# Optimization experiments

Measured on AMD Instinct MI355X. Metric: run time of the kernel, lower is better.

Reference implementation:

```python
import jax, jax.numpy as jnp
import numpy as np
from jax import lax

SR = 4      # sr_prior
LAM = 0.1   # lam

# ---- MATLAB-style bicubic imresize (as used by the DRP repo's imresize) ----

def _cubic(x):
    ax = np.abs(x); ax2 = ax * ax; ax3 = ax2 * ax
    return ((1.5 * ax3 - 2.5 * ax2 + 1.0) * (ax <= 1)
            + (-0.5 * ax3 + 2.5 * ax2 - 4.0 * ax + 2.0) * ((ax > 1) & (ax <= 2)))

def _resize_matrix(in_len, out_len, scale):
    """Dense (out_len, in_len) bicubic resize matrix with antialiasing on downscale."""
    kw = 4.0
    if scale < 1.0:
        kw = kw / scale  # antialias: widen kernel
    x = np.arange(1, out_len + 1, dtype=np.float64)
    u = x / scale + 0.5 * (1.0 - 1.0 / scale)
    left = np.floor(u - kw / 2.0)
    P = int(np.ceil(kw)) + 2
    ind = left[:, None] + np.arange(P)[None, :]
    if scale < 1.0:
        w = scale * _cubic(scale * (u[:, None] - ind))
    else:
        w = _cubic(u[:, None] - ind)
    w = w / w.sum(axis=1, keepdims=True)
    # mirror boundary handling (MATLAB imresize)
    aux = np.concatenate([np.arange(in_len), np.arange(in_len - 1, -1, -1)])
    idx = aux[np.mod(ind.astype(np.int64) - 1, aux.size)]
    W = np.zeros((out_len, in_len), dtype=np.float64)
    rows = np.repeat(np.arange(out_len), P)
    np.add.at(W, (rows, idx.ravel()), w.ravel())
    return W.astype(np.float32)

def _imresize(img, scale):
    # img: (C, H, W) -> (C, H*scale, W*scale), separable matrix form
    C, H, W = img.shape
    oh, ow = int(round(H * scale)), int(round(W * scale))
    Wh = jnp.asarray(_resize_matrix(H, oh, scale))
    Ww = jnp.asarray(_resize_matrix(W, ow, scale))
    t = jnp.einsum('oi,cij->coj', Wh, img)      # resize rows
    return jnp.einsum('pj,coj->cop', Ww, t)     # resize cols

def _wrap_corr(x, k):
    """Cross-correlate (C,H,W) with 2D kernel k under circular ('wrap') padding."""
    ph, pw = k.shape[0] // 2, k.shape[1] // 2
    xp = jnp.pad(x, ((0, 0), (ph, ph), (pw, pw)), mode='wrap')
    y = lax.conv_general_dilated(xp[:, None, :, :], k[None, None, :, :], (1, 1), 'VALID')
    return y[:, 0]


def setup_inputs() -> dict:
    key = jax.random.key(0)
    k1, k2 = jax.random.split(key)
    im = jax.random.normal(k1, (1, 3, 2048, 2048), dtype=jnp.float32)
    kernel = jax.random.uniform(k2, (25, 25), dtype=jnp.float32)
    kernel = kernel / kernel.sum()  # normalized blur PSF
    return {"im": im, "kernel": kernel}


def reference(im, kernel):
    x = im[0]  # (C, H, W)
    # ndimage.convolve(x, k, wrap)  == correlate with flipped kernel
    ax = _wrap_corr(x, kernel[::-1, ::-1])
    # ndimage.convolve(ax, k[::-1,::-1], wrap) == correlate with k (adjoint A^T)
    atax = _wrap_corr(ax, kernel)
    hx = _imresize(x, 1.0 / SR)       # H x: downsample
    hthx = _imresize(hx, float(SR))   # H^T(ish): upsample back
    return (atax + LAM * hthx)[None]  # (1, C, H, W)
```

## Files before the change

kernel.cpp:

```cpp
#include <hip/hip_runtime.h>

static constexpr int IMG  = 2048;
static constexpr int CH   = 3;
static constexpr int KS   = 25;
static constexpr int HALO = 12;
static constexpr int DN   = 512;
static constexpr int PD   = 18;
static constexpr int PU   = 6;
static constexpr float LAM = 0.1f;

__device__ __forceinline__ double cubic_d(double x) {
  double ax = fabs(x), ax2 = ax * ax, ax3 = ax2 * ax;
  if (ax <= 1.0) return 1.5 * ax3 - 2.5 * ax2 + 1.0;
  if (ax <= 2.0) return -0.5 * ax3 + 2.5 * ax2 - 4.0 * ax + 2.0;
  return 0.0;
}

__global__ void build_tables(float* dwW, int* dwI, float* uwW, int* uwI) {
  int i = blockIdx.x * blockDim.x + threadIdx.x;
  if (i < DN) {
    const double scale = 0.25;
    double u = (double)(i + 1) / scale + 0.5 * (1.0 - 1.0 / scale);
    double left = floor(u - 8.0);
    double w[PD]; int id[PD]; double s = 0.0;
    for (int p = 0; p < PD; ++p) {
      double ind = left + p;
      w[p] = scale * cubic_d(scale * (u - ind));
      s += w[p];
      long long m = ((long long)ind - 1) % (2 * IMG);
      if (m < 0) m += 2 * IMG;
      id[p] = (m < IMG) ? (int)m : (int)(2 * IMG - 1 - m);
    }
    for (int p = 0; p < PD; ++p) {
      dwW[i * PD + p] = (float)(w[p] / s);
      dwI[i * PD + p] = id[p];
    }
  }
  if (i < IMG) {
    const double scale = 4.0;
    double u = (double)(i + 1) / scale + 0.5 * (1.0 - 1.0 / scale);
    double left = floor(u - 2.0);
    double w[PU]; int id[PU]; double s = 0.0;
    for (int p = 0; p < PU; ++p) {
      double ind = left + p;
      w[p] = cubic_d(u - ind);
      s += w[p];
      long long m = ((long long)ind - 1) % (2 * DN);
      if (m < 0) m += 2 * DN;
      id[p] = (m < DN) ? (int)m : (int)(2 * DN - 1 - m);
    }
    for (int p = 0; p < PU; ++p) {
      uwW[i * PU + p] = (float)(w[p] / s);
      uwI[i * PU + p] = id[p];
    }
  }
}

template <int FLIP>
__global__ __launch_bounds__(256, 4) void corr25(const float* __restrict__ src,
                                                 const float* __restrict__ kw,
                                                 float* __restrict__ dst) {
  constexpr int TW = 128, TH = 32;
  constexpr int SW = 160;
  constexpr int SH = TH + KS - 1;
  constexpr int CHUNKS = 152 / 4;
  __shared__ float tile[SH][SW];

  const int tid = threadIdx.x;
  const int c   = blockIdx.z;
  const int x0  = blockIdx.x * TW;
  const int y0  = blockIdx.y * TH;
  const float* s = src + (size_t)c * IMG * IMG;

  const bool xwrap = (x0 < HALO) || (x0 + TW + HALO > IMG);
  for (int ci = tid; ci < SH * CHUNKS; ci += 256) {
    int r  = ci / CHUNKS;
    int cj = ci - r * CHUNKS;
    int gy = (y0 + r - HALO) & (IMG - 1);
    int col  = 4 * cj;
    int scol = col ^ (((r >> 1) & 7) << 2);
    float4 v;
    if (!xwrap) {
      v = *reinterpret_cast<const float4*>(&s[(size_t)gy * IMG + (x0 - HALO + col)]);
    } else {
      int gx = x0 - HALO + col;
      v.x = s[(size_t)gy * IMG + ((gx + 0) & (IMG - 1))];
      v.y = s[(size_t)gy * IMG + ((gx + 1) & (IMG - 1))];
      v.z = s[(size_t)gy * IMG + ((gx + 2) & (IMG - 1))];
      v.w = s[(size_t)gy * IMG + ((gx + 3) & (IMG - 1))];
    }
    *reinterpret_cast<float4*>(&tile[r][scol]) = v;
  }
  __syncthreads();

  const int tx    = tid & 15;
  const int tyt   = tid >> 4;
  const int ox    = tx * 8;
  const int rbase = tyt * 2;

  float acc0[8], acc1[8];
#pragma unroll
  for (int o = 0; o < 8; ++o) { acc0[o] = 0.f; acc1[o] = 0.f; }

#pragma unroll 2
  for (int rr = 0; rr < KS + 1; ++rr) {
    const int r   = rbase + rr;
    const int swz = ((r >> 1) & 7) << 2;
    float row[32];
#pragma unroll
    for (int j = 0; j < 8; ++j) {
      float4 v = *reinterpret_cast<const float4*>(&tile[r][(ox + 4 * j) ^ swz]);
      row[4 * j + 0] = v.x; row[4 * j + 1] = v.y;
      row[4 * j + 2] = v.z; row[4 * j + 3] = v.w;
    }
    if (rr <= KS - 1) {
      const int ky = rr;
#pragma unroll
      for (int kx = 0; kx < KS; ++kx) {
        float w = FLIP ? kw[(KS - 1 - ky) * KS + (KS - 1 - kx)]
                       : kw[ky * KS + kx];
#pragma unroll
        for (int o = 0; o < 8; ++o) acc0[o] = fmaf(w, row[kx + o], acc0[o]);
      }
    }
    if (rr >= 1) {
      const int ky = rr - 1;
#pragma unroll
      for (int kx = 0; kx < KS; ++kx) {
        float w = FLIP ? kw[(KS - 1 - ky) * KS + (KS - 1 - kx)]
                       : kw[ky * KS + kx];
#pragma unroll
        for (int o = 0; o < 8; ++o) acc1[o] = fmaf(w, row[kx + o], acc1[o]);
      }
    }
  }

  float* d0 = dst + (size_t)c * IMG * IMG + (size_t)(y0 + rbase) * IMG + x0 + ox;
  *reinterpret_cast<float4*>(d0)           = make_float4(acc0[0], acc0[1], acc0[2], acc0[3]);
  *reinterpret_cast<float4*>(d0 + 4)       = make_float4(acc0[4], acc0[5], acc0[6], acc0[7]);
  *reinterpret_cast<float4*>(d0 + IMG)     = make_float4(acc1[0], acc1[1], acc1[2], acc1[3]);
  *reinterpret_cast<float4*>(d0 + IMG + 4) = make_float4(acc1[4], acc1[5], acc1[6], acc1[7]);
}

__global__ void rows_down(const float* __restrict__ src, float* __restrict__ dst,
                          const float* __restrict__ wW, const int* __restrict__ wI) {
  int x = blockIdx.x * blockDim.x + threadIdx.x;
  int o = blockIdx.y;
  int c = blockIdx.z;
  const float* s = src + (size_t)c * IMG * IMG;
  float acc = 0.f;
#pragma unroll
  for (int p = 0; p < PD; ++p)
    acc = fmaf(wW[o * PD + p], s[(size_t)wI[o * PD + p] * IMG + x], acc);
  dst[((size_t)c * DN + o) * IMG + x] = acc;
}

__global__ void cols_down(const float* __restrict__ src, float* __restrict__ dst,
                          const float* __restrict__ wW, const int* __restrict__ wI) {
  int o = blockIdx.x * blockDim.x + threadIdx.x;
  int y = blockIdx.y;
  int c = blockIdx.z;
  const float* s = src + ((size_t)c * DN + y) * IMG;
  float acc = 0.f;
#pragma unroll
  for (int p = 0; p < PD; ++p)
    acc = fmaf(wW[o * PD + p], s[wI[o * PD + p]], acc);
  dst[((size_t)c * DN + y) * DN + o] = acc;
}

__global__ void rows_up(const float* __restrict__ src, float* __restrict__ dst,
                        const float* __restrict__ wW, const int* __restrict__ wI) {
  int x = blockIdx.x * blockDim.x + threadIdx.x;
  int o = blockIdx.y;
  int c = blockIdx.z;
  const float* s = src + (size_t)c * DN * DN;
  float acc = 0.f;
#pragma unroll
  for (int p = 0; p < PU; ++p)
    acc = fmaf(wW[o * PU + p], s[(size_t)wI[o * PU + p] * DN + x], acc);
  dst[((size_t)c * IMG + o) * DN + x] = acc;
}

__global__ void cols_up_add(const float* __restrict__ src, float* __restrict__ out,
                            const float* __restrict__ wW, const int* __restrict__ wI) {
  int x = blockIdx.x * blockDim.x + threadIdx.x;
  int y = blockIdx.y;
  int c = blockIdx.z;
  const float* s = src + ((size_t)c * IMG + y) * DN;
  float acc = 0.f;
#pragma unroll
  for (int p = 0; p < PU; ++p)
    acc = fmaf(wW[x * PU + p], s[wI[x * PU + p]], acc);
  size_t oi = ((size_t)c * IMG + y) * IMG + x;
  out[oi] = fmaf(LAM, acc, out[oi]);
}

extern "C" void kernel_launch(void* const* d_in, const int* in_sizes, int n_in,
                              void* d_out, int out_size, void* d_ws, size_t ws_size,
                              hipStream_t stream) {
  const float* im  = (const float*)d_in[0];
  const float* ker = (const float*)d_in[1];
  float* out = (float*)d_out;
  float* ws  = (float*)d_ws;

  const size_t NIM = (size_t)CH * IMG * IMG;

  float* ax = ws;
  float* t1 = ws;
  float* t2 = t1 + (size_t)CH * DN * IMG;
  float* t3 = t2 + (size_t)CH * DN * DN;
  float* dwW = ws + NIM;
  int*   dwI = (int*)(dwW + DN * PD);
  float* uwW = (float*)(dwI + DN * PD);
  int*   uwI = (int*)(uwW + (size_t)IMG * PU);

  build_tables<<<(IMG + 255) / 256, 256, 0, stream>>>(dwW, dwI, uwW, uwI);

  dim3 cgrid(IMG / 128, IMG / 32, CH);
  corr25<1><<<cgrid, 256, 0, stream>>>(im, ker, ax);
  corr25<0><<<cgrid, 256, 0, stream>>>(ax, ker, out);

  rows_down  <<<dim3(IMG / 256, DN,  CH), 256, 0, stream>>>(im, t1, dwW, dwI);
  cols_down  <<<dim3(DN  / 256, DN,  CH), 256, 0, stream>>>(t1, t2, dwW, dwI);
  rows_up    <<<dim3(DN  / 256, IMG, CH), 256, 0, stream>>>(t2, t3, uwW, uwI);
  cols_up_add<<<dim3(IMG / 256, IMG, CH), 256, 0, stream>>>(t3, out, uwW, uwI);
}
```

Measured before the change: 471.9 us.

## Register-block four output rows per thread and double-buffer LDS strip loads

The 25x25 correlation tile grows from 32 to 64 rows, and each thread now accumulates 4 output rows instead of 2. Each loaded LDS strip therefore feeds up to four accumulator rows, which cuts shared-memory reads and halo overhead per output. Strip loads are double-buffered so the next row is fetched while FMAs run on the current one, and the LDS swizzle is adjusted to the new row grouping. In exchange, register pressure rises and launch bounds drop to 2 blocks per CU, which lowers occupancy.

```diff
diff --git a/kernel.cpp b/kernel.cpp
--- a/kernel.cpp
+++ b/kernel.cpp
@@ -57,13 +57,14 @@
 }
 
 template <int FLIP>
-__global__ __launch_bounds__(256, 4) void corr25(const float* __restrict__ src,
-                                                 const float* __restrict__ kw,
+__global__ __launch_bounds__(256, 2) void corr25(const float* __restrict__ src,
+                                                 const float* __restrict__ kwp,
                                                  float* __restrict__ dst) {
-  constexpr int TW = 128, TH = 32;
+  constexpr int TW = 128, TH = 64;
   constexpr int SW = 160;
   constexpr int SH = TH + KS - 1;
   constexpr int CHUNKS = 152 / 4;
+  constexpr int NSTRIP = 4 + KS - 1;
   __shared__ float tile[SH][SW];
 
   const int tid = threadIdx.x;
@@ -78,7 +79,7 @@
     int cj = ci - r * CHUNKS;
     int gy = (y0 + r - HALO) & (IMG - 1);
     int col  = 4 * cj;
-    int scol = col ^ (((r >> 1) & 7) << 2);
+    int scol = col ^ (((r >> 2) & 7) << 2);
     float4 v;
     if (!xwrap) {
       v = *reinterpret_cast<const float4*>(&s[(size_t)gy * IMG + (x0 - HALO + col)]);
@@ -96,50 +97,63 @@
   const int tx    = tid & 15;
   const int tyt   = tid >> 4;
   const int ox    = tx * 8;
-  const int rbase = tyt * 2;
-
-  float acc0[8], acc1[8];
-#pragma unroll
-  for (int o = 0; o < 8; ++o) { acc0[o] = 0.f; acc1[o] = 0.f; }
-
-#pragma unroll 2
-  for (int rr = 0; rr < KS + 1; ++rr) {
-    const int r   = rbase + rr;
-    const int swz = ((r >> 1) & 7) << 2;
-    float row[32];
-#pragma unroll
-    for (int j = 0; j < 8; ++j) {
-      float4 v = *reinterpret_cast<const float4*>(&tile[r][(ox + 4 * j) ^ swz]);
-      row[4 * j + 0] = v.x; row[4 * j + 1] = v.y;
-      row[4 * j + 2] = v.z; row[4 * j + 3] = v.w;
-    }
-    if (rr <= KS - 1) {
-      const int ky = rr;
-#pragma unroll
-      for (int kx = 0; kx < KS; ++kx) {
-        float w = FLIP ? kw[(KS - 1 - ky) * KS + (KS - 1 - kx)]
-                       : kw[ky * KS + kx];
-#pragma unroll
-        for (int o = 0; o < 8; ++o) acc0[o] = fmaf(w, row[kx + o], acc0[o]);
-      }
-    }
-    if (rr >= 1) {
-      const int ky = rr - 1;
-#pragma unroll
-      for (int kx = 0; kx < KS; ++kx) {
-        float w = FLIP ? kw[(KS - 1 - ky) * KS + (KS - 1 - kx)]
-                       : kw[ky * KS + kx];
-#pragma unroll
-        for (int o = 0; o < 8; ++o) acc1[o] = fmaf(w, row[kx + o], acc1[o]);
-      }
-    }
-  }
+  const int rbase = tyt * 4;
+
+  float acc[4][8];
+#pragma unroll
+  for (int dy = 0; dy < 4; ++dy)
+#pragma unroll
+    for (int o = 0; o < 8; ++o) acc[dy][o] = 0.f;
+
+#define LOADSTRIP(BUF, R)                                                     \
+  do {                                                                        \
+    const int _r   = (R);                                                     \
+    const int _swz = ((_r >> 2) & 7) << 2;                                    \
+    _Pragma("unroll")                                                         \
+    for (int j = 0; j < 8; ++j)                                               \
+      BUF[j] = *reinterpret_cast<const float4*>(&tile[_r][(ox + 4 * j) ^ _swz]); \
+  } while (0)
+
+#define DOFMA(BUF, RR)                                                        \
+  do {                                                                        \
+    const float* _row = reinterpret_cast<const float*>(BUF);                  \
+    const int _rr = (RR);                                                     \
+    _Pragma("unroll")                                                         \
+    for (int dy = 0; dy < 4; ++dy) {                                          \
+      const int _ky = _rr - dy;                                               \
+      if (_ky >= 0 && _ky < KS) {                                             \
+        _Pragma("unroll")                                                     \
+        for (int kx = 0; kx < KS; ++kx) {                                     \
+          float _w = FLIP ? kwp[(KS - 1 - _ky) * KS + (KS - 1 - kx)]          \
+                          : kwp[_ky * KS + kx];                               \
+          _Pragma("unroll")                                                   \
+          for (int o = 0; o < 8; ++o)                                         \
+            acc[dy][o] = fmaf(_w, _row[kx + o], acc[dy][o]);                  \
+        }                                                                     \
+      }                                                                       \
+    }                                                                         \
+  } while (0)
+
+  float4 bufA[8], bufB[8];
+  LOADSTRIP(bufA, rbase);
+#pragma unroll 1
+  for (int rr = 0; rr < NSTRIP; rr += 2) {
+    LOADSTRIP(bufB, rbase + rr + 1);
+    DOFMA(bufA, rr);
+    if (rr + 2 < NSTRIP) LOADSTRIP(bufA, rbase + rr + 2);
+    DOFMA(bufB, rr + 1);
+  }
+#undef LOADSTRIP
+#undef DOFMA
 
   float* d0 = dst + (size_t)c * IMG * IMG + (size_t)(y0 + rbase) * IMG + x0 + ox;
-  *reinterpret_cast<float4*>(d0)           = make_float4(acc0[0], acc0[1], acc0[2], acc0[3]);
-  *reinterpret_cast<float4*>(d0 + 4)       = make_float4(acc0[4], acc0[5], acc0[6], acc0[7]);
-  *reinterpret_cast<float4*>(d0 + IMG)     = make_float4(acc1[0], acc1[1], acc1[2], acc1[3]);
-  *reinterpret_cast<float4*>(d0 + IMG + 4) = make_float4(acc1[4], acc1[5], acc1[6], acc1[7]);
+#pragma unroll
+  for (int dy = 0; dy < 4; ++dy) {
+    *reinterpret_cast<float4*>(d0 + (size_t)dy * IMG) =
+        make_float4(acc[dy][0], acc[dy][1], acc[dy][2], acc[dy][3]);
+    *reinterpret_cast<float4*>(d0 + (size_t)dy * IMG + 4) =
+        make_float4(acc[dy][4], acc[dy][5], acc[dy][6], acc[dy][7]);
+  }
 }
 
 __global__ void rows_down(const float* __restrict__ src, float* __restrict__ dst,
@@ -216,7 +230,7 @@
 
   build_tables<<<(IMG + 255) / 256, 256, 0, stream>>>(dwW, dwI, uwW, uwI);
 
-  dim3 cgrid(IMG / 128, IMG / 32, CH);
+  dim3 cgrid(IMG / 128, IMG / 64, CH);
   corr25<1><<<cgrid, 256, 0, stream>>>(im, ker, ax);
   corr25<0><<<cgrid, 256, 0, stream>>>(ax, ker, out);
 
```

After: 503.1 us. +6.6%, slower.
